# Kernel optimization log

Measured on AMD Instinct MI355X. Metric: run time of the kernel, lower is better.

Reference implementation:

```python
import jax, jax.numpy as jnp
import numpy as np

B, L, C, D = 32, 256, 16, 128
WORD_VOCAB, CHR_VOCAB = 50000, 128


def conv1d(x, w, b):
    # x: [N, D, T], w: [D_out, D_in, 3], torch Conv1d (cross-correlation), padding=1
    y = jax.lax.conv_general_dilated(x, w, window_strides=(1,), padding=[(1, 1)],
                                     dimension_numbers=('NCH', 'OIH', 'NCH'))
    return y + b[None, :, None]


def setup_inputs() -> dict:
    key = jax.random.key(0)
    k1, k2, k3, k4, k5, k6, k7, k8 = jax.random.split(key, 8)
    word_vector = jax.random.randint(k1, (B, L), 0, WORD_VOCAB)
    words_in_char = jax.random.randint(k2, (B, L, C), 0, CHR_VOCAB)
    # embedding tables, padding_idx=0 -> row 0 is zeros
    word_table = (jax.random.normal(k3, (WORD_VOCAB, D), jnp.float32) * 0.02).at[0].set(0.0)
    chr_table = (jax.random.normal(k4, (CHR_VOCAB, D), jnp.float32) * 0.02).at[0].set(0.0)
    scale = 1.0 / np.sqrt(D * 3)
    conv_chr_w = jax.random.normal(k5, (D, D, 3), jnp.float32) * scale
    conv_chr_b = jax.random.normal(k6, (D,), jnp.float32) * scale
    conv_word_w = jax.random.normal(k7, (D, D, 3), jnp.float32) * scale
    conv_word_b = jax.random.normal(k8, (D,), jnp.float32) * scale
    return dict(word_vector=word_vector, words_in_char=words_in_char,
                word_table=word_table, chr_table=chr_table,
                conv_chr_w=conv_chr_w, conv_chr_b=conv_chr_b,
                conv_word_w=conv_word_w, conv_word_b=conv_word_b)


def reference(word_vector, words_in_char, word_table, chr_table,
              conv_chr_w, conv_chr_b, conv_word_w, conv_word_b):
    # --- char path (batched version of the per-word Python loop) ---
    chr_emb = chr_table[words_in_char]                       # [B, L, C, D]
    x = chr_emb.reshape(B * L, C, D).transpose(0, 2, 1)      # [B*L, D, C]
    word_conv = conv1d(x, conv_chr_w, conv_chr_b)            # [B*L, D, C]
    char_feats = word_conv.max(axis=2).reshape(B, L, D)      # max over char positions
    # --- word path ---
    word_emb = word_table[word_vector]                       # [B, L, D]
    out = conv1d(word_emb.transpose(0, 2, 1), conv_word_w, conv_word_b)  # [B, D, L]
    # stack both branch outputs into one array: [2, B, D, L]
    return jnp.stack([out, char_feats.transpose(0, 2, 1)])
```

## Files before the change

kernel.cpp:

```cpp
#include <hip/hip_runtime.h>

typedef __attribute__((ext_vector_type(8))) short short8;
typedef __attribute__((ext_vector_type(4))) float float4_t;

#define NB 32
#define NL 256
#define ND 128
#define OUT_PLANE (NB * ND * NL)
#define XS 136
#define FR_WORD 49152
#define CHRB 98304

__device__ inline unsigned short f2bf(float f) {
    union { float f; unsigned int i; } c;
    c.f = f;
    unsigned int r = c.i + 0x7FFFu + ((c.i >> 16) & 1u);
    return (unsigned short)(r >> 16);
}

__global__ void make_frags(const float* __restrict__ Wc,
                           const float* __restrict__ Ww,
                           const float* __restrict__ chrT,
                           unsigned short* __restrict__ out) {
    int i = blockIdx.x * 256 + threadIdx.x;
    if (i < CHRB) {
        const float* W = (i < FR_WORD) ? Wc : Ww;
        int ii = (i < FR_WORD) ? i : i - FR_WORD;
        int j    = ii & 7;
        int lane = (ii >> 3) & 63;
        int nt   = (ii >> 9) & 7;
        int s    = ii >> 12;
        int dout = nt * 16 + (lane & 15);
        int t    = s >> 2;
        int k    = (s & 3) * 32 + ((lane >> 4) & 3) * 8 + j;
        out[i] = f2bf(W[(dout * 128 + k) * 3 + t]);
    } else {
        int j = i - CHRB;
        out[i] = f2bf(chrT[j]);
    }
}

__device__ __forceinline__ void mfma12(const unsigned short* __restrict__ buf,
                                       const short8 bfrag[12][4],
                                       int m, int quad, float4_t acc[4]) {
#pragma unroll
    for (int p = 0; p < 4; ++p) acc[p] = (float4_t){0.f, 0.f, 0.f, 0.f};
#pragma unroll
    for (int s = 0; s < 12; ++s) {
        short8 a = *(const short8*)&buf[(m + (s >> 2)) * XS +
                                        (s & 3) * 32 + quad * 8];
#pragma unroll
        for (int p = 0; p < 4; ++p)
            acc[p] = __builtin_amdgcn_mfma_f32_16x16x32_bf16(
                a, bfrag[s][p], acc[p], 0, 0, 0);
    }
}

__global__ __launch_bounds__(128, 2) void conv_kernel(
    const int* __restrict__ wv, const int* __restrict__ wic,
    const float* __restrict__ wordT,
    const unsigned short* __restrict__ ws,
    const float* __restrict__ biasC, const float* __restrict__ biasW,
    float* __restrict__ out) {
    __shared__ unsigned short X[4][18 * XS];
    const int tid  = threadIdx.x;
    const int wave = tid >> 6, lane = tid & 63;
    const int m = lane & 15, quad = lane >> 4;
    const int bid = blockIdx.x;

    if (bid >= 512) {
        const unsigned short* chrB = ws + CHRB;
        const int w0 = (bid - 512) * 8;
        const int b = w0 >> 8, l0 = w0 & 255;
        short8 bfrag[12][4];
#pragma unroll
        for (int s = 0; s < 12; ++s)
#pragma unroll
            for (int p = 0; p < 4; ++p)
                bfrag[s][p] = *(const short8*)(
                    ws + (((s * 8 + wave * 4 + p) * 64 + lane) << 3));
        float bb[4];
#pragma unroll
        for (int p = 0; p < 4; ++p) bb[p] = biasC[wave * 64 + p * 16 + m];

        for (int p = tid; p < XS; p += 128)
#pragma unroll
            for (int q = 0; q < 4; ++q) { X[q][p] = 0; X[q][17 * XS + p] = 0; }

        const int ra = tid >> 4, sub = tid & 15;

#pragma unroll
        for (int q = 0; q < 2; ++q) {
            int j0 = wic[(w0 + q) * 16 + ra];
            int j1 = wic[(w0 + q) * 16 + ra + 8];
            short8 g0 = *(const short8*)(chrB + j0 * 128 + sub * 8);
            short8 g1 = *(const short8*)(chrB + j1 * 128 + sub * 8);
            *(short8*)&X[q][(ra + 1) * XS + sub * 8] = g0;
            *(short8*)&X[q][(ra + 9) * XS + sub * 8] = g1;
        }
        int iA0 = wic[(w0 + 2) * 16 + ra];
        int iA1 = wic[(w0 + 2) * 16 + ra + 8];
        int iC0 = wic[(w0 + 3) * 16 + ra];
        int iC1 = wic[(w0 + 3) * 16 + ra + 8];
        __syncthreads();

        float v[4][4];
#pragma unroll
        for (int j = 0; j < 8; j += 2) {
            short8 g0, g1;
            if (j < 6) {
                g0 = *(const short8*)(chrB + iA0 * 128 + sub * 8);
                g1 = *(const short8*)(chrB + iA1 * 128 + sub * 8);
            }

            float4_t acc[4];
            mfma12(X[j & 3], bfrag, m, quad, acc);

            short8 h0, h1;
            if (j < 6) {
                *(short8*)&X[(j + 2) & 3][(ra + 1) * XS + sub * 8] = g0;
                *(short8*)&X[(j + 2) & 3][(ra + 9) * XS + sub * 8] = g1;
                h0 = *(const short8*)(chrB + iC0 * 128 + sub * 8);
                h1 = *(const short8*)(chrB + iC1 * 128 + sub * 8);
                if (j < 4) {
                    iA0 = wic[(w0 + j + 4) * 16 + ra];
                    iA1 = wic[(w0 + j + 4) * 16 + ra + 8];
                    iC0 = wic[(w0 + j + 5) * 16 + ra];
                    iC1 = wic[(w0 + j + 5) * 16 + ra + 8];
                }
            }

#pragma unroll
            for (int p = 0; p < 4; ++p) {
                float t = fmaxf(fmaxf(acc[p].x, acc[p].y),
                                fmaxf(acc[p].z, acc[p].w));
                t = fmaxf(t, __shfl_xor(t, 16, 64));
                t = fmaxf(t, __shfl_xor(t, 32, 64));
                v[p][j & 3] = t + bb[p];
            }

            mfma12(X[(j + 1) & 3], bfrag, m, quad, acc);

            if (j < 6) {
                *(short8*)&X[(j + 3) & 3][(ra + 1) * XS + sub * 8] = h0;
                *(short8*)&X[(j + 3) & 3][(ra + 9) * XS + sub * 8] = h1;
            }

#pragma unroll
            for (int p = 0; p < 4; ++p) {
                float t = fmaxf(fmaxf(acc[p].x, acc[p].y),
                                fmaxf(acc[p].z, acc[p].w));
                t = fmaxf(t, __shfl_xor(t, 16, 64));
                t = fmaxf(t, __shfl_xor(t, 32, 64));
                v[p][(j + 1) & 3] = t + bb[p];
            }
            if (((j + 1) & 3) == 3 && quad == 0) {
                float* obase = out + OUT_PLANE + b * (ND * NL) + l0 + (j & 4);
#pragma unroll
                for (int p = 0; p < 4; ++p) {
                    float4_t pk = {v[p][0], v[p][1], v[p][2], v[p][3]};
                    *(float4_t*)&obase[(wave * 64 + p * 16 + m) * NL] = pk;
                }
            }
            __syncthreads();
        }
    } else {
        const int b = bid >> 4, l0 = (bid & 15) << 4;
        short8 bfrag[12][4];
#pragma unroll
        for (int s = 0; s < 12; ++s)
#pragma unroll
            for (int p = 0; p < 4; ++p)
                bfrag[s][p] = *(const short8*)(
                    ws + FR_WORD + (((s * 8 + wave * 4 + p) * 64 + lane) << 3));
        float bb[4];
#pragma unroll
        for (int p = 0; p < 4; ++p) bb[p] = biasW[wave * 64 + p * 16 + m];

#pragma unroll
        for (int i0 = 0; i0 < 2; ++i0) {
            int i = tid + i0 * 128;
            if (i < 144) {
                int rr = i >> 3, sg = i & 7;
                int l = l0 + rr - 1;
                int idx = (l >= 0 && l < NL) ? wv[b * NL + l] : 0;
                const float4_t* src =
                    (const float4_t*)(wordT + idx * 128 + sg * 16);
                float4_t f0 = src[0], f1 = src[1], f2 = src[2], f3 = src[3];
                unsigned short t16[16];
                t16[0]=f2bf(f0.x); t16[1]=f2bf(f0.y); t16[2]=f2bf(f0.z); t16[3]=f2bf(f0.w);
                t16[4]=f2bf(f1.x); t16[5]=f2bf(f1.y); t16[6]=f2bf(f1.z); t16[7]=f2bf(f1.w);
                t16[8]=f2bf(f2.x); t16[9]=f2bf(f2.y); t16[10]=f2bf(f2.z); t16[11]=f2bf(f2.w);
                t16[12]=f2bf(f3.x); t16[13]=f2bf(f3.y); t16[14]=f2bf(f3.z); t16[15]=f2bf(f3.w);
                *(short8*)&X[0][rr * XS + sg * 16]     = *(const short8*)&t16[0];
                *(short8*)&X[0][rr * XS + sg * 16 + 8] = *(const short8*)&t16[8];
            }
        }
        __syncthreads();

        float4_t acc[4];
#pragma unroll
        for (int p = 0; p < 4; ++p) acc[p] = (float4_t){0.f, 0.f, 0.f, 0.f};
#pragma unroll
        for (int s = 0; s < 12; ++s) {
            short8 a = *(const short8*)&X[0][(m + (s >> 2)) * XS +
                                            (s & 3) * 32 + quad * 8];
#pragma unroll
            for (int p = 0; p < 4; ++p)
                acc[p] = __builtin_amdgcn_mfma_f32_16x16x32_bf16(
                    a, bfrag[s][p], acc[p], 0, 0, 0);
        }

        float* obase = out + b * (ND * NL) + l0 + quad * 4;
#pragma unroll
        for (int p = 0; p < 4; ++p) {
            int dout = wave * 64 + p * 16 + m;
            float4_t pk;
            pk.x = acc[p].x + bb[p];
            pk.y = acc[p].y + bb[p];
            pk.z = acc[p].z + bb[p];
            pk.w = acc[p].w + bb[p];
            *(float4_t*)&obase[dout * NL] = pk;
        }
    }
}

extern "C" void kernel_launch(void* const* d_in, const int* in_sizes, int n_in,
                              void* d_out, int out_size, void* d_ws,
                              size_t ws_size, hipStream_t stream) {
    const int* word_vector   = (const int*)d_in[0];
    const int* words_in_char = (const int*)d_in[1];
    const float* word_table  = (const float*)d_in[2];
    const float* chr_table   = (const float*)d_in[3];
    const float* conv_chr_w  = (const float*)d_in[4];
    const float* conv_chr_b  = (const float*)d_in[5];
    const float* conv_word_w = (const float*)d_in[6];
    const float* conv_word_b = (const float*)d_in[7];
    float* out            = (float*)d_out;
    unsigned short* wsp   = (unsigned short*)d_ws;

    make_frags<<<448, 256, 0, stream>>>(conv_chr_w, conv_word_w, chr_table, wsp);
    conv_kernel<<<1536, 128, 0, stream>>>(word_vector, words_in_char,
                                          word_table, wsp,
                                          conv_chr_b, conv_word_b, out);
}
```

Baseline: 106.2 us.

## Switch char-path conv to 32x32x16 MFMA processing two words per tile

```diff
diff --git a/kernel.cpp b/kernel.cpp
--- a/kernel.cpp
+++ b/kernel.cpp
@@ -1,13 +1,16 @@
 #include <hip/hip_runtime.h>
 
 typedef __attribute__((ext_vector_type(8))) short short8;
+typedef __attribute__((ext_vector_type(2))) float float2_t;
 typedef __attribute__((ext_vector_type(4))) float float4_t;
+typedef __attribute__((ext_vector_type(16))) float float16_t;
 
 #define NB 32
 #define NL 256
 #define ND 128
 #define OUT_PLANE (NB * ND * NL)
 #define XS 136
+#define BUFSZ (18 * XS)
 #define FR_WORD 49152
 #define CHRB 98304
 
@@ -23,9 +26,18 @@
                            const float* __restrict__ chrT,
                            unsigned short* __restrict__ out) {
     int i = blockIdx.x * 256 + threadIdx.x;
-    if (i < CHRB) {
-        const float* W = (i < FR_WORD) ? Wc : Ww;
-        int ii = (i < FR_WORD) ? i : i - FR_WORD;
+    if (i < FR_WORD) {
+        int j    = i & 7;
+        int lane = (i >> 3) & 63;
+        int nt   = (i >> 9) & 3;
+        int s    = i >> 11;
+        int dout = nt * 32 + (lane & 31);
+        int kk   = s * 16 + ((lane >> 5) & 1) * 8 + j;
+        int t    = kk >> 7;
+        int d    = kk & 127;
+        out[i] = f2bf(Wc[(dout * 128 + d) * 3 + t]);
+    } else if (i < CHRB) {
+        int ii = i - FR_WORD;
         int j    = ii & 7;
         int lane = (ii >> 3) & 63;
         int nt   = (ii >> 9) & 7;
@@ -33,26 +45,10 @@
         int dout = nt * 16 + (lane & 15);
         int t    = s >> 2;
         int k    = (s & 3) * 32 + ((lane >> 4) & 3) * 8 + j;
-        out[i] = f2bf(W[(dout * 128 + k) * 3 + t]);
+        out[i] = f2bf(Ww[(dout * 128 + k) * 3 + t]);
     } else {
         int j = i - CHRB;
         out[i] = f2bf(chrT[j]);
-    }
-}
-
-__device__ __forceinline__ void mfma12(const unsigned short* __restrict__ buf,
-                                       const short8 bfrag[12][4],
-                                       int m, int quad, float4_t acc[4]) {
-#pragma unroll
-    for (int p = 0; p < 4; ++p) acc[p] = (float4_t){0.f, 0.f, 0.f, 0.f};
-#pragma unroll
-    for (int s = 0; s < 12; ++s) {
-        short8 a = *(const short8*)&buf[(m + (s >> 2)) * XS +
-                                        (s & 3) * 32 + quad * 8];
-#pragma unroll
-        for (int p = 0; p < 4; ++p)
-            acc[p] = __builtin_amdgcn_mfma_f32_16x16x32_bf16(
-                a, bfrag[s][p], acc[p], 0, 0, 0);
     }
 }
 
@@ -62,26 +58,27 @@
     const unsigned short* __restrict__ ws,
     const float* __restrict__ biasC, const float* __restrict__ biasW,
     float* __restrict__ out) {
-    __shared__ unsigned short X[4][18 * XS];
+    __shared__ unsigned short X[4][BUFSZ];
     const int tid  = threadIdx.x;
     const int wave = tid >> 6, lane = tid & 63;
-    const int m = lane & 15, quad = lane >> 4;
     const int bid = blockIdx.x;
 
     if (bid >= 512) {
         const unsigned short* chrB = ws + CHRB;
         const int w0 = (bid - 512) * 8;
         const int b = w0 >> 8, l0 = w0 & 255;
-        short8 bfrag[12][4];
-#pragma unroll
-        for (int s = 0; s < 12; ++s)
-#pragma unroll
-            for (int p = 0; p < 4; ++p)
+        const int n32 = lane & 31;
+        const int h   = (lane >> 5) & 1;
+        const int r15 = lane & 15;
+        const int wsel = (lane >> 4) & 1;
+
+        short8 bfrag[24][2];
+#pragma unroll
+        for (int s = 0; s < 24; ++s)
+#pragma unroll
+            for (int p = 0; p < 2; ++p)
                 bfrag[s][p] = *(const short8*)(
-                    ws + (((s * 8 + wave * 4 + p) * 64 + lane) << 3));
-        float bb[4];
-#pragma unroll
-        for (int p = 0; p < 4; ++p) bb[p] = biasC[wave * 64 + p * 16 + m];
+                    ws + (((s * 4 + wave * 2 + p) * 64 + lane) << 3));
 
         for (int p = tid; p < XS; p += 128)
 #pragma unroll
@@ -104,17 +101,31 @@
         int iC1 = wic[(w0 + 3) * 16 + ra + 8];
         __syncthreads();
 
-        float v[4][4];
 #pragma unroll
         for (int j = 0; j < 8; j += 2) {
+            const unsigned short* abuf = X[(j + wsel) & 3];
+
             short8 g0, g1;
             if (j < 6) {
                 g0 = *(const short8*)(chrB + iA0 * 128 + sub * 8);
                 g1 = *(const short8*)(chrB + iA1 * 128 + sub * 8);
             }
 
-            float4_t acc[4];
-            mfma12(X[j & 3], bfrag, m, quad, acc);
+            float16_t acc[2];
+#pragma unroll
+            for (int p = 0; p < 2; ++p)
+#pragma unroll
+                for (int e = 0; e < 16; ++e) acc[p][e] = 0.f;
+
+#pragma unroll
+            for (int s = 0; s < 12; ++s) {
+                short8 a = *(const short8*)&abuf[(r15 + (s >> 3)) * XS +
+                                                 (s & 7) * 16 + h * 8];
+#pragma unroll
+                for (int p = 0; p < 2; ++p)
+                    acc[p] = __builtin_amdgcn_mfma_f32_32x32x16_bf16(
+                        a, bfrag[s][p], acc[p], 0, 0, 0);
+            }
 
             short8 h0, h1;
             if (j < 6) {
@@ -131,15 +142,14 @@
             }
 
 #pragma unroll
-            for (int p = 0; p < 4; ++p) {
-                float t = fmaxf(fmaxf(acc[p].x, acc[p].y),
-                                fmaxf(acc[p].z, acc[p].w));
-                t = fmaxf(t, __shfl_xor(t, 16, 64));
-                t = fmaxf(t, __shfl_xor(t, 32, 64));
-                v[p][j & 3] = t + bb[p];
-            }
-
-            mfma12(X[(j + 1) & 3], bfrag, m, quad, acc);
+            for (int s = 12; s < 24; ++s) {
+                short8 a = *(const short8*)&abuf[(r15 + (s >> 3)) * XS +
+                                                 (s & 7) * 16 + h * 8];
+#pragma unroll
+                for (int p = 0; p < 2; ++p)
+                    acc[p] = __builtin_amdgcn_mfma_f32_32x32x16_bf16(
+                        a, bfrag[s][p], acc[p], 0, 0, 0);
+            }
 
             if (j < 6) {
                 *(short8*)&X[(j + 3) & 3][(ra + 1) * XS + sub * 8] = h0;
@@ -147,24 +157,27 @@
             }
 
 #pragma unroll
-            for (int p = 0; p < 4; ++p) {
-                float t = fmaxf(fmaxf(acc[p].x, acc[p].y),
-                                fmaxf(acc[p].z, acc[p].w));
-                t = fmaxf(t, __shfl_xor(t, 16, 64));
-                t = fmaxf(t, __shfl_xor(t, 32, 64));
-                v[p][(j + 1) & 3] = t + bb[p];
-            }
-            if (((j + 1) & 3) == 3 && quad == 0) {
-                float* obase = out + OUT_PLANE + b * (ND * NL) + l0 + (j & 4);
-#pragma unroll
-                for (int p = 0; p < 4; ++p) {
-                    float4_t pk = {v[p][0], v[p][1], v[p][2], v[p][3]};
-                    *(float4_t*)&obase[(wave * 64 + p * 16 + m) * NL] = pk;
+            for (int p = 0; p < 2; ++p) {
+                float v0 = acc[p][0], v1 = acc[p][8];
+#pragma unroll
+                for (int e = 1; e < 8; ++e) {
+                    v0 = fmaxf(v0, acc[p][e]);
+                    v1 = fmaxf(v1, acc[p][e + 8]);
                 }
+                v0 = fmaxf(v0, __shfl_xor(v0, 32, 64));
+                v1 = fmaxf(v1, __shfl_xor(v1, 32, 64));
+                int dout = wave * 64 + p * 32 + n32;
+                if (lane < 32) {
+                    float bc = biasC[dout];
+                    float2_t st = {v0 + bc, v1 + bc};
+                    *(float2_t*)&out[OUT_PLANE + b * (ND * NL) + dout * NL +
+                                     l0 + j] = st;
+                }
             }
             __syncthreads();
         }
     } else {
+        const int m = lane & 15, quad = lane >> 4;
         const int b = bid >> 4, l0 = (bid & 15) << 4;
         short8 bfrag[12][4];
 #pragma unroll
```

Result: no change. 105.4 us (-0.7%).
